# Performance work log

Hardware: AMD Instinct MI355X
Metric: run time of the kernel (lower is better)

The kernel has to match this reference:

```python
import jax, jax.numpy as jnp
import numpy as np

P_EPS = 1e-6            # nn.PairwiseDistance default eps
ALPHA = 0.25
STD_TARGET = 1.0
NUM_COMMUNITIES = 512   # C = number of unique community ids
BIG = 1e30              # masking value for hard-negative min


def setup_inputs() -> dict:
    key = jax.random.key(0)
    k1, k2, k3 = jax.random.split(key, 3)
    B, N, D, C = 1, 100000, 128, NUM_COMMUNITIES
    node_features = jax.random.normal(k1, (B, N, D), dtype=jnp.float32)
    # row 0: a permutation of node indices; row 1: community of that node.
    perm = jax.random.permutation(k2, N).astype(jnp.int32)
    comm_per_node = jnp.concatenate([
        jnp.arange(C, dtype=jnp.int32),  # guarantee every community appears
        jax.random.randint(k3, (N - C,), 0, C, dtype=jnp.int32),
    ])
    community_belong_list = jnp.stack([perm, comm_per_node[perm]])  # [2, N]
    return {"node_features": node_features, "community_belong_list": community_belong_list}


def reference(node_features, community_belong_list):
    B, N, D = node_features.shape
    C = NUM_COMMUNITIES
    dt = node_features.dtype

    # ---- _community_inverse_permute: invert row-0 permutation, reorder columns ----
    perm = community_belong_list[0]
    inv = jnp.zeros((N,), perm.dtype).at[perm].add(jnp.arange(N, dtype=perm.dtype))
    cbl = community_belong_list[:, inv]          # row0 == arange(N) after this
    comm = cbl[1]                                # [N] community id per node
    src = node_features[:, cbl[0], :]            # [B,N,D] gather (identity order)

    # ---- groupby sum / count -> community means ----
    comm_sum = jnp.zeros((B, C, D), dt).at[:, comm, :].add(src)        # [B,C,D]
    counts = jnp.zeros((C,), dt).at[comm].add(jnp.asarray(1.0, dt))   # [C]
    comm_mean = comm_sum / counts[None, :, None]                      # [B,C,D]

    # ---- cdist(node_features, comm_mean, p=2) -> [B,N,C] ----
    x2 = jnp.sum(node_features * node_features, -1)                   # [B,N]
    c2 = jnp.sum(comm_mean * comm_mean, -1)                           # [B,C]
    dots = jnp.einsum('bnd,bcd->bnc', node_features, comm_mean)
    distance = jnp.sqrt(jnp.maximum(x2[:, :, None] + c2[:, None, :] - 2.0 * dots, 0.0))

    # ---- leave-one-out community mean per node, positive distance ----
    cnt_pn = counts[comm]                                             # [N]
    cnt_m1 = jnp.maximum(cnt_pn - 1.0, 1.0)                           # [N]
    x_minus = jnp.where((cnt_pn == 1.0)[None, :, None], jnp.asarray(0.0, dt), src)
    loo_mean = (comm_sum[:, comm, :] - x_minus) / cnt_m1[None, :, None]
    pos_dist = jnp.sqrt(jnp.sum((loo_mean - src + P_EPS) ** 2, -1))   # [B,N]

    # ---- negatives: all communities except the node's own ----
    own = distance[:, jnp.arange(N), comm]                            # [B,N]
    mean_neg = (jnp.sum(distance, -1) - own) / (C - 1)                # [B,N]
    pos_mask = jnp.zeros((N, C), bool).at[jnp.arange(N), comm].set(True)
    hard_neg = jnp.min(jnp.where(pos_mask[None], jnp.asarray(BIG, dt), distance), -1)

    trip_mean = jnp.maximum(pos_dist - mean_neg + ALPHA, 0.0)
    trip_min = jnp.maximum(pos_dist - hard_neg + ALPHA, 0.0)

    # ---- groupby std (unbiased) per community per feature ----
    sq = jnp.zeros((B, C, D), dt).at[:, comm, :].add((src - comm_mean[:, comm, :]) ** 2)
    std = jnp.sqrt(sq / jnp.maximum(counts - 1.0, 1.0)[None, :, None])

    return (trip_mean.mean(), trip_min.mean(), ((std - STD_TARGET) ** 2).mean())
```

## Files before the change

kernel.cpp:

```cpp
#include <hip/hip_runtime.h>

#define NCOMM 512
#define DIM   128
#define ALPHA 0.25f
#define PEPS  1e-6f
#define BIGF  1e30f
#define TILE_C 16
#define NT    (NCOMM / TILE_C)

typedef __attribute__((ext_vector_type(8))) _Float16 f16x8;
typedef __attribute__((ext_vector_type(4))) float f32x4;

#define GLOAD_LDS16(g, l) __builtin_amdgcn_global_load_lds( \
    (const __attribute__((address_space(1))) void*)(g), \
    (__attribute__((address_space(3))) void*)(l), 16, 0, 0)


__global__ void k_prep(const int* __restrict__ cbl, int* __restrict__ comm,
                       int* __restrict__ counts, int N) {
    __shared__ int h[NCOMM];
    int t = threadIdx.x;
    h[t] = 0; h[t + 256] = 0;
    __syncthreads();
    int i = blockIdx.x * 256 + t;
    if (i < N) {
        int p = cbl[i];
        int c = cbl[N + i];
        comm[p] = c;
        atomicAdd(&h[c], 1);
    }
    __syncthreads();
    int v = h[t];        if (v) atomicAdd(&counts[t], v);
    v = h[t + 256];      if (v) atomicAdd(&counts[t + 256], v);
}

__global__ void k_scan(const int* __restrict__ counts, int* __restrict__ offsets,
                       int* __restrict__ cursor, float* __restrict__ countf) {
    __shared__ int sc[NCOMM];
    int t = threadIdx.x;
    int v0 = counts[t];
    sc[t] = v0;
    __syncthreads();
    for (int off = 1; off < NCOMM; off <<= 1) {
        int v = (t >= off) ? sc[t - off] : 0;
        __syncthreads();
        sc[t] += v;
        __syncthreads();
    }
    int excl = sc[t] - v0;
    offsets[t] = excl;
    cursor[t]  = excl;
    countf[t]  = (float)v0;
}

__global__ void k_sort(const int* __restrict__ comm, int* __restrict__ cursor,
                       int* __restrict__ sorted, int N) {
    __shared__ int h[NCOMM], hb[NCOMM];
    int t = threadIdx.x;
    h[t] = 0; h[t + 256] = 0;
    __syncthreads();
    int j0 = blockIdx.x * 1024 + t;
    int cs[4];
    #pragma unroll
    for (int q = 0; q < 4; ++q) {
        int j = j0 + q * 256;
        cs[q] = (j < N) ? comm[j] : -1;
        if (cs[q] >= 0) atomicAdd(&h[cs[q]], 1);
    }
    __syncthreads();
    int v = h[t];        if (v) hb[t] = atomicAdd(&cursor[t], v);
    v = h[t + 256];      if (v) hb[t + 256] = atomicAdd(&cursor[t + 256], v);
    __syncthreads();
    #pragma unroll
    for (int q = 0; q < 4; ++q) {
        int j = j0 + q * 256;
        if (cs[q] >= 0) {
            int p = atomicAdd(&hb[cs[q]], 1);
            sorted[p] = j;
        }
    }
}


__global__ void __launch_bounds__(512) k_stats(
        const float* __restrict__ NF,
        const int* __restrict__ sorted, const int* __restrict__ offsets,
        const int* __restrict__ counts,
        float* __restrict__ comm_sum,
        _Float16* __restrict__ CMh,
        float* __restrict__ c2, float* __restrict__ accum) {
    __shared__ int ridx[512];
    __shared__ float4 bufS[512], bufQ[512];
    int c = blockIdx.x, t = threadIdx.x;
    int d4 = t & 31, r = t >> 5;
    int cnt = counts[c], base = offsets[c];
    const float4* NF4 = (const float4*)NF;

    float4 s4 = make_float4(0.f, 0.f, 0.f, 0.f);
    float4 q4 = make_float4(0.f, 0.f, 0.f, 0.f);
    for (int chunk = 0; chunk < cnt; chunk += 512) {
        int m = min(cnt - chunk, 512);
        for (int i = t; i < m; i += 512) ridx[i] = sorted[base + chunk + i];
        __syncthreads();
        int i = r;
        for (; i + 48 < m; i += 64) {
            int a0 = ridx[i], a1 = ridx[i + 16], a2 = ridx[i + 32], a3 = ridx[i + 48];
            float4 v0 = NF4[(size_t)a0 * 32 + d4];
            float4 v1 = NF4[(size_t)a1 * 32 + d4];
            float4 v2 = NF4[(size_t)a2 * 32 + d4];
            float4 v3 = NF4[(size_t)a3 * 32 + d4];
            s4.x += v0.x; s4.y += v0.y; s4.z += v0.z; s4.w += v0.w;
            q4.x = fmaf(v0.x, v0.x, q4.x); q4.y = fmaf(v0.y, v0.y, q4.y);
            q4.z = fmaf(v0.z, v0.z, q4.z); q4.w = fmaf(v0.w, v0.w, q4.w);
            s4.x += v1.x; s4.y += v1.y; s4.z += v1.z; s4.w += v1.w;
            q4.x = fmaf(v1.x, v1.x, q4.x); q4.y = fmaf(v1.y, v1.y, q4.y);
            q4.z = fmaf(v1.z, v1.z, q4.z); q4.w = fmaf(v1.w, v1.w, q4.w);
            s4.x += v2.x; s4.y += v2.y; s4.z += v2.z; s4.w += v2.w;
            q4.x = fmaf(v2.x, v2.x, q4.x); q4.y = fmaf(v2.y, v2.y, q4.y);
            q4.z = fmaf(v2.z, v2.z, q4.z); q4.w = fmaf(v2.w, v2.w, q4.w);
            s4.x += v3.x; s4.y += v3.y; s4.z += v3.z; s4.w += v3.w;
            q4.x = fmaf(v3.x, v3.x, q4.x); q4.y = fmaf(v3.y, v3.y, q4.y);
            q4.z = fmaf(v3.z, v3.z, q4.z); q4.w = fmaf(v3.w, v3.w, q4.w);
        }
        for (; i < m; i += 16) {
            float4 v = NF4[(size_t)ridx[i] * 32 + d4];
            s4.x += v.x; s4.y += v.y; s4.z += v.z; s4.w += v.w;
            q4.x = fmaf(v.x, v.x, q4.x); q4.y = fmaf(v.y, v.y, q4.y);
            q4.z = fmaf(v.z, v.z, q4.z); q4.w = fmaf(v.w, v.w, q4.w);
        }
        __syncthreads();
    }
    bufS[t] = s4; bufQ[t] = q4;
    __syncthreads();
    if (t < 256) {
        float4 a = bufS[t], b = bufS[t + 256];
        a.x += b.x; a.y += b.y; a.z += b.z; a.w += b.w; bufS[t] = a;
        float4 e = bufQ[t], f = bufQ[t + 256];
        e.x += f.x; e.y += f.y; e.z += f.z; e.w += f.w; bufQ[t] = e;
    }
    __syncthreads();
    if (t < 128) {
        float4 a = bufS[t], b = bufS[t + 128];
        a.x += b.x; a.y += b.y; a.z += b.z; a.w += b.w; bufS[t] = a;
        float4 e = bufQ[t], f = bufQ[t + 128];
        e.x += f.x; e.y += f.y; e.z += f.z; e.w += f.w; bufQ[t] = e;
    }
    __syncthreads();
    if (t < 64) {
        float4 a = bufS[t], b = bufS[t + 64];
        a.x += b.x; a.y += b.y; a.z += b.z; a.w += b.w; bufS[t] = a;
        float4 e = bufQ[t], f = bufQ[t + 64];
        e.x += f.x; e.y += f.y; e.z += f.z; e.w += f.w; bufQ[t] = e;
    }
    __syncthreads();
    if (t < 32) {
        float4 a = bufS[t], b = bufS[t + 32];
        a.x += b.x; a.y += b.y; a.z += b.z; a.w += b.w;
        float4 e = bufQ[t], f = bufQ[t + 32];
        e.x += f.x; e.y += f.y; e.z += f.z; e.w += f.w;
        float sarr[4] = {a.x, a.y, a.z, a.w};
        float qarr[4] = {e.x, e.y, e.z, e.w};
        float cf = (float)cnt;
        float mm = 0.f, ee = 0.f;
        #pragma unroll
        for (int k = 0; k < 4; ++k) {
            int d = t * 4 + k;
            float s = sarr[k];
            comm_sum[c * DIM + d] = s;
            float m = (cnt > 0) ? s / cf : 0.f;
            CMh[c * DIM + d] = (_Float16)m;
            float varn = fmaxf(fmaf(-cf * m, m, qarr[k]), 0.f);
            float stdv = sqrtf(varn / fmaxf(cf - 1.f, 1.f));
            float er = stdv - 1.f;
            mm = fmaf(m, m, mm);
            ee = fmaf(er, er, ee);
        }
        #pragma unroll
        for (int msk = 1; msk < 32; msk <<= 1) {
            mm += __shfl_xor(mm, msk);
            ee += __shfl_xor(ee, msk);
        }
        if (t == 0) {
            c2[c] = mm;
            atomicAdd(&accum[2], ee);
        }
    }
}


__global__ void __launch_bounds__(256, 4) k_main(
        const float* __restrict__ NF,
        const _Float16* __restrict__ CMh,
        const float* __restrict__ comm_sum,
        const float* __restrict__ c2g,
        const float* __restrict__ countf,
        const int* __restrict__ comm,
        float* __restrict__ accum, int N) {
    __shared__ _Float16 Bst[4][4][TILE_C * 64];
    __shared__ float c2s[NCOMM];
    __shared__ int   comms[128];
    __shared__ float x2sh[128];
    __shared__ float sums[128], mins[128];
    __shared__ float red[8];

    int tid = threadIdx.x;
    int w  = tid >> 6;
    int l  = tid & 63;
    int lr = l & 15;
    int lk = l >> 4;
    int n0 = blockIdx.x * 128;

    int off0 = ((l >> 3) << 7) + (((l & 7) ^ ((l >> 3) & 7)) << 3);
    const _Float16* gsrc = CMh + off0;
    auto stage = [&](int ss, int b) {
        const _Float16* g = gsrc + (size_t)(ss >> 1) * 2048 + (ss & 1) * 64;
        _Float16* lh = &Bst[w][b][0];
        GLOAD_LDS16(g,        lh);
        GLOAD_LDS16(g + 1024, lh + 512);
    };
    stage(0, 0); stage(1, 1); stage(2, 2);

    c2s[tid]       = c2g[tid];
    c2s[tid + 256] = c2g[tid + 256];
    if (tid < 128) {
        int gn = n0 + tid;
        comms[tid] = (gn < N) ? comm[gn] : -1;
    }

    f16x8 ah[2][4];
    #pragma unroll
    for (int mf = 0; mf < 2; ++mf) {
        int n = n0 + w * 32 + mf * 16 + lr;
        const float4* src = (const float4*)NF + (size_t)n * 32 + lk * 2;
        float p2 = 0.f;
        #pragma unroll
        for (int ks = 0; ks < 4; ++ks) {
            float4 v0 = make_float4(0.f, 0.f, 0.f, 0.f), v1 = v0;
            if (n < N) { v0 = src[ks * 8]; v1 = src[ks * 8 + 1]; }
            float fr[8] = {v0.x, v0.y, v0.z, v0.w, v1.x, v1.y, v1.z, v1.w};
            f16x8 hh;
            #pragma unroll
            for (int t = 0; t < 8; ++t) {
                hh[t] = (_Float16)fr[t];
                p2 = fmaf(fr[t], fr[t], p2);
            }
            ah[mf][ks] = hh;
        }
        p2 += __shfl_xor(p2, 16);
        p2 += __shfl_xor(p2, 32);
        if (lk == 0) x2sh[w * 32 + mf * 16 + lr] = -0.5f * p2;
    }
    __syncthreads();

    f32x4 x2v[2];
    int cnv[2][4];
    float sumv[2][4], minv[2][4];
    #pragma unroll
    for (int mf = 0; mf < 2; ++mf) {
        x2v[mf] = *(const f32x4*)&x2sh[w * 32 + mf * 16 + lk * 4];
        #pragma unroll
        for (int j = 0; j < 4; ++j) {
            cnv[mf][j] = comms[w * 32 + mf * 16 + lk * 4 + j];
            sumv[mf][j] = 0.f; minv[mf][j] = BIGF;
        }
    }

    for (int tt = 0; tt < NT; ++tt) {
        f32x4 acc0, acc1;
        {
            int ssn = 2 * tt + 3;
            if (ssn < 64) stage(ssn, ssn & 3);
            if (tt <= 30) { asm volatile("s_waitcnt vmcnt(6)" ::: "memory"); }
            else          { asm volatile("s_waitcnt vmcnt(2)" ::: "memory"); }
            __builtin_amdgcn_sched_barrier(0);
            const _Float16* bp = &Bst[w][(2 * tt) & 3][0];
            acc0 = x2v[0]; acc1 = x2v[1];
            #pragma unroll
            for (int ks2 = 0; ks2 < 2; ++ks2) {
                int ch = (ks2 * 4 + lk) ^ (lr & 7);
                f16x8 b = *(const f16x8*)&bp[(size_t)(lr * 64 + ch * 8)];
                acc0 = __builtin_amdgcn_mfma_f32_16x16x32_f16(ah[0][ks2], b, acc0, 0, 0, 0);
                acc1 = __builtin_amdgcn_mfma_f32_16x16x32_f16(ah[1][ks2], b, acc1, 0, 0, 0);
            }
        }
        {
            int ssn = 2 * tt + 4;
            if (ssn < 64) stage(ssn, ssn & 3);
            if (tt <= 29)      { asm volatile("s_waitcnt vmcnt(6)" ::: "memory"); }
            else if (tt == 30) { asm volatile("s_waitcnt vmcnt(4)" ::: "memory"); }
            else               { asm volatile("s_waitcnt vmcnt(0)" ::: "memory"); }
            __builtin_amdgcn_sched_barrier(0);
            const _Float16* bp = &Bst[w][(2 * tt + 1) & 3][0];
            #pragma unroll
            for (int ks2 = 0; ks2 < 2; ++ks2) {
                int ch = (ks2 * 4 + lk) ^ (lr & 7);
                f16x8 b = *(const f16x8*)&bp[(size_t)(lr * 64 + ch * 8)];
                acc0 = __builtin_amdgcn_mfma_f32_16x16x32_f16(ah[0][2 + ks2], b, acc0, 0, 0, 0);
                acc1 = __builtin_amdgcn_mfma_f32_16x16x32_f16(ah[1][2 + ks2], b, acc1, 0, 0, 0);
            }
            int ccol = tt * TILE_C + lr;
            float c2v = c2s[ccol];
            #pragma unroll
            for (int j = 0; j < 4; ++j) {
                float d2a = fmaf(-2.f, acc0[j], c2v);
                float da  = __builtin_amdgcn_sqrtf(fmaxf(d2a, 0.f));
                sumv[0][j] += da;
                minv[0][j] = fminf(minv[0][j], (cnv[0][j] == ccol) ? BIGF : da);
                float d2b = fmaf(-2.f, acc1[j], c2v);
                float db  = __builtin_amdgcn_sqrtf(fmaxf(d2b, 0.f));
                sumv[1][j] += db;
                minv[1][j] = fminf(minv[1][j], (cnv[1][j] == ccol) ? BIGF : db);
            }
        }
    }

    #pragma unroll
    for (int mf = 0; mf < 2; ++mf)
        #pragma unroll
        for (int j = 0; j < 4; ++j) {
            float sv = sumv[mf][j], mv = minv[mf][j];
            #pragma unroll
            for (int msk = 1; msk < 16; msk <<= 1) {
                sv += __shfl_xor(sv, msk);
                mv = fminf(mv, __shfl_xor(mv, msk));
            }
            if (lr == 0) {
                int idx = w * 32 + mf * 16 + lk * 4 + j;
                sums[idx] = sv; mins[idx] = mv;
            }
        }
    __syncthreads();

    float tmean = 0.f, tminv = 0.f;
    {
        int ln = tid >> 1, half = tid & 1;
        int n = n0 + ln;
        if (n < N) {
            int cnode = comms[ln];
            float cf  = countf[cnode];
            float cm1 = fmaxf(cf - 1.f, 1.f);
            float rs  = 1.f / cm1;
            bool single = (cf == 1.f);
            const float4* srow = (const float4*)NF + (size_t)n * 32 + half * 16;
            const float4* csum = (const float4*)(comm_sum + (size_t)cnode * DIM) + half * 16;
            float q = 0.f, dot = 0.f;
            #pragma unroll
            for (int m = 0; m < 16; ++m) {
                float4 sv = srow[m];
                float4 cs = csum[m];
                float4 xm = single ? make_float4(0.f, 0.f, 0.f, 0.f) : sv;
                float lx = (cs.x - xm.x) * rs - sv.x + PEPS;
                float ly = (cs.y - xm.y) * rs - sv.y + PEPS;
                float lz = (cs.z - xm.z) * rs - sv.z + PEPS;
                float lw = (cs.w - xm.w) * rs - sv.w + PEPS;
                q = fmaf(lx, lx, fmaf(ly, ly, fmaf(lz, lz, fmaf(lw, lw, q))));
                dot = fmaf(sv.x, cs.x, fmaf(sv.y, cs.y, fmaf(sv.z, cs.z, fmaf(sv.w, cs.w, dot))));
            }
            q   += __shfl_xor(q, 1);
            dot += __shfl_xor(dot, 1);
            if (half == 0) {
                float pos = sqrtf(q);
                float x2 = -2.f * x2sh[ln];
                float ownd2 = x2 + c2s[cnode] - 2.f * (dot / cf);
                float own = sqrtf(fmaxf(ownd2, 0.f));
                float mean_neg = (sums[ln] - own) * (1.f / (float)(NCOMM - 1));
                tmean = fmaxf(pos - mean_neg + ALPHA, 0.f);
                tminv = fmaxf(pos - mins[ln] + ALPHA, 0.f);
            }
        }
    }
    #pragma unroll
    for (int msk = 1; msk < 64; msk <<= 1) {
        tmean += __shfl_xor(tmean, msk);
        tminv += __shfl_xor(tminv, msk);
    }
    if ((tid & 63) == 0) { red[w * 2] = tmean; red[w * 2 + 1] = tminv; }
    __syncthreads();
    if (tid == 0) {
        atomicAdd(&accum[0], red[0] + red[2] + red[4] + red[6]);
        atomicAdd(&accum[1], red[1] + red[3] + red[5] + red[7]);
    }
}

__global__ void k_final(const float* __restrict__ accum, float* __restrict__ out, int N) {
    if (threadIdx.x == 0) {
        out[0] = accum[0] / (float)N;
        out[1] = accum[1] / (float)N;
        out[2] = accum[2] / (float)(NCOMM * DIM);
    }
}


extern "C" void kernel_launch(void* const* d_in, const int* in_sizes, int n_in,
                              void* d_out, int out_size, void* d_ws, size_t ws_size,
                              hipStream_t stream) {
    const float* NF  = (const float*)d_in[0];
    const int*   CBL = (const int*)d_in[1];
    int N = in_sizes[1] / 2;
    if (N <= 0) return;

    char* ws = (char*)d_ws;
    float* accum   = (float*)ws;
    int*   counts  = (int*)(ws + 16);
    int*   cursor  = (int*)(ws + 16 + 2048);
    int*   offsets = (int*)(ws + 16 + 2 * 2048);
    float* countf  = (float*)(ws + 16 + 3 * 2048);
    float* c2      = (float*)(ws + 16 + 4 * 2048);
    char* p = ws + 16 + 5 * 2048;
    int* comm   = (int*)p; p += (size_t)N * 4;
    int* sorted = (int*)p; p += (size_t)N * 4;
    float* comm_sum = (float*)p; p += (size_t)NCOMM * DIM * 4;
    _Float16* CMh = (_Float16*)p;

    hipMemsetAsync(d_ws, 0, 16 + 2048, stream);

    int nb = (N + 255) / 256;
    k_prep<<<nb, 256, 0, stream>>>(CBL, comm, counts, N);
    k_scan<<<1, NCOMM, 0, stream>>>(counts, offsets, cursor, countf);
    int nb4 = (N + 1023) / 1024;
    k_sort<<<nb4, 256, 0, stream>>>(comm, cursor, sorted, N);
    k_stats<<<NCOMM, 512, 0, stream>>>(NF, sorted, offsets, counts,
                                       comm_sum, CMh, c2, accum);
    int mb = (N + 127) / 128;
    k_main<<<mb, 256, 0, stream>>>(NF, CMh, comm_sum, c2, countf,
                                   comm, accum, N);
    k_final<<<1, 64, 0, stream>>>(accum, (float*)d_out, N);
}
```

Measured before the change: 119.7 us.

## Make k_main persistent with register-resident centroids and double-buffered node tiles

Turns k_main into a persistent kernel of 256 blocks with 1024 threads each. Each of the 16 waves keeps its own 32-community slice of the fp16 centroid matrix in registers. Node tiles of 64 rows are staged through double-buffered LDS, with the next tile prefetched while the current one is processed. The goal is to stop re-streaming all 512 centroids from global memory to LDS for every 128-node block. The cost is an extra cross-wave partial-sum reduction through LDS and two block barriers per tile. Launch_bounds(1024,4) also puts pressure on registers and occupancy.

```diff
diff --git a/kernel.cpp b/kernel.cpp
--- a/kernel.cpp
+++ b/kernel.cpp
@@ -5,15 +5,9 @@
 #define ALPHA 0.25f
 #define PEPS  1e-6f
 #define BIGF  1e30f
-#define TILE_C 16
-#define NT    (NCOMM / TILE_C)
 
 typedef __attribute__((ext_vector_type(8))) _Float16 f16x8;
 typedef __attribute__((ext_vector_type(4))) float f32x4;
-
-#define GLOAD_LDS16(g, l) __builtin_amdgcn_global_load_lds( \
-    (const __attribute__((address_space(1))) void*)(g), \
-    (__attribute__((address_space(3))) void*)(l), 16, 0, 0)
 
 
 __global__ void k_prep(const int* __restrict__ cbl, int* __restrict__ comm,
@@ -188,7 +182,7 @@
 }
 
 
-__global__ void __launch_bounds__(256, 4) k_main(
+__global__ void __launch_bounds__(1024, 4) k_main(
         const float* __restrict__ NF,
         const _Float16* __restrict__ CMh,
         const float* __restrict__ comm_sum,
@@ -196,189 +190,193 @@
         const float* __restrict__ countf,
         const int* __restrict__ comm,
         float* __restrict__ accum, int N) {
-    __shared__ _Float16 Bst[4][4][TILE_C * 64];
+    __shared__ _Float16 Ast[2][64 * DIM];
+    __shared__ float part_s[64][16];
+    __shared__ float part_m[64][16];
     __shared__ float c2s[NCOMM];
-    __shared__ int   comms[128];
-    __shared__ float x2sh[128];
-    __shared__ float sums[128], mins[128];
-    __shared__ float red[8];
+    __shared__ float x2t[2][64];
+    __shared__ int   comt[2][64];
+    __shared__ float red[32];
 
     int tid = threadIdx.x;
     int w  = tid >> 6;
     int l  = tid & 63;
     int lr = l & 15;
     int lk = l >> 4;
-    int n0 = blockIdx.x * 128;
-
-    int off0 = ((l >> 3) << 7) + (((l & 7) ^ ((l >> 3) & 7)) << 3);
-    const _Float16* gsrc = CMh + off0;
-    auto stage = [&](int ss, int b) {
-        const _Float16* g = gsrc + (size_t)(ss >> 1) * 2048 + (ss & 1) * 64;
-        _Float16* lh = &Bst[w][b][0];
-        GLOAD_LDS16(g,        lh);
-        GLOAD_LDS16(g + 1024, lh + 512);
-    };
-    stage(0, 0); stage(1, 1); stage(2, 2);
-
-    c2s[tid]       = c2g[tid];
-    c2s[tid + 256] = c2g[tid + 256];
-    if (tid < 128) {
-        int gn = n0 + tid;
-        comms[tid] = (gn < N) ? comm[gn] : -1;
-    }
-
-    f16x8 ah[2][4];
+    int row = tid >> 4;
+    int cq  = tid & 15;
+    int TT  = (N + 63) >> 6;
+
+    f16x8 bh[2][4];
     #pragma unroll
-    for (int mf = 0; mf < 2; ++mf) {
-        int n = n0 + w * 32 + mf * 16 + lr;
-        const float4* src = (const float4*)NF + (size_t)n * 32 + lk * 2;
-        float p2 = 0.f;
-        #pragma unroll
-        for (int ks = 0; ks < 4; ++ks) {
-            float4 v0 = make_float4(0.f, 0.f, 0.f, 0.f), v1 = v0;
-            if (n < N) { v0 = src[ks * 8]; v1 = src[ks * 8 + 1]; }
-            float fr[8] = {v0.x, v0.y, v0.z, v0.w, v1.x, v1.y, v1.z, v1.w};
-            f16x8 hh;
+    for (int s = 0; s < 2; ++s) {
+        int c0 = w * 32 + s * 16;
+        #pragma unroll
+        for (int ks = 0; ks < 4; ++ks)
+            bh[s][ks] = *(const f16x8*)&CMh[(size_t)(c0 + lr) * DIM + ks * 32 + lk * 8];
+    }
+    if (tid < NCOMM) c2s[tid] = c2g[tid];
+
+    {
+        int n = blockIdx.x * 64 + row;
+        const float4* base = (const float4*)NF + (size_t)n * 32 + cq * 2;
+        float4 v0 = make_float4(0.f, 0.f, 0.f, 0.f), v1 = v0;
+        int cm = -1;
+        if (n < N) { v0 = base[0]; v1 = base[1]; cm = comm[n]; }
+        float fr[8] = {v0.x, v0.y, v0.z, v0.w, v1.x, v1.y, v1.z, v1.w};
+        f16x8 hh; float p2 = 0.f;
+        #pragma unroll
+        for (int u = 0; u < 8; ++u) { hh[u] = (_Float16)fr[u]; p2 = fmaf(fr[u], fr[u], p2); }
+        *(f16x8*)&Ast[0][row * DIM + ((cq ^ (row & 7)) * 8)] = hh;
+        p2 += __shfl_xor(p2, 1); p2 += __shfl_xor(p2, 2);
+        p2 += __shfl_xor(p2, 4); p2 += __shfl_xor(p2, 8);
+        if (cq == 0) x2t[0][row] = -0.5f * p2;
+        if (cq == 1) comt[0][row] = cm;
+    }
+    __syncthreads();
+
+    float tmean = 0.f, tminv = 0.f;
+    int cur = 0;
+    for (int t = blockIdx.x; t < TT; t += 256) {
+        int tn = t + 256;
+        bool hasNext = tn < TT;
+        float4 nv0 = make_float4(0.f, 0.f, 0.f, 0.f), nv1 = nv0;
+        int ncm = -1;
+        if (hasNext) {
+            int n = tn * 64 + row;
+            const float4* base = (const float4*)NF + (size_t)n * 32 + cq * 2;
+            if (n < N) { nv0 = base[0]; nv1 = base[1]; ncm = comm[n]; }
+        }
+
+        float sumv[4][4], minv[4][4];
+        #pragma unroll
+        for (int nf = 0; nf < 4; ++nf)
             #pragma unroll
-            for (int t = 0; t < 8; ++t) {
-                hh[t] = (_Float16)fr[t];
-                p2 = fmaf(fr[t], fr[t], p2);
+            for (int j = 0; j < 4; ++j) { sumv[nf][j] = 0.f; minv[nf][j] = BIGF; }
+
+        const _Float16* Ab = &Ast[cur][0];
+        #pragma unroll
+        for (int nf = 0; nf < 4; ++nf) {
+            int rbase = (nf * 16 + lr) * DIM;
+            f16x8 ah0 = *(const f16x8*)&Ab[rbase + (((0 + lk) ^ (lr & 7)) * 8)];
+            f16x8 ah1 = *(const f16x8*)&Ab[rbase + (((4 + lk) ^ (lr & 7)) * 8)];
+            f16x8 ah2 = *(const f16x8*)&Ab[rbase + (((8 + lk) ^ (lr & 7)) * 8)];
+            f16x8 ah3 = *(const f16x8*)&Ab[rbase + (((12 + lk) ^ (lr & 7)) * 8)];
+            f32x4 x2v = *(const f32x4*)&x2t[cur][nf * 16 + lk * 4];
+            int4  cn  = *(const int4*)&comt[cur][nf * 16 + lk * 4];
+            #pragma unroll
+            for (int s = 0; s < 2; ++s) {
+                f32x4 acc = x2v;
+                acc = __builtin_amdgcn_mfma_f32_16x16x32_f16(ah0, bh[s][0], acc, 0, 0, 0);
+                acc = __builtin_amdgcn_mfma_f32_16x16x32_f16(ah1, bh[s][1], acc, 0, 0, 0);
+                acc = __builtin_amdgcn_mfma_f32_16x16x32_f16(ah2, bh[s][2], acc, 0, 0, 0);
+                acc = __builtin_amdgcn_mfma_f32_16x16x32_f16(ah3, bh[s][3], acc, 0, 0, 0);
+                int ccol = w * 32 + s * 16 + lr;
+                float c2v = c2s[ccol];
+                int cna[4] = {cn.x, cn.y, cn.z, cn.w};
+                #pragma unroll
+                for (int j = 0; j < 4; ++j) {
+                    float d2 = fmaf(-2.f, acc[j], c2v);
+                    float da = __builtin_amdgcn_sqrtf(fmaxf(d2, 0.f));
+                    sumv[nf][j] += da;
+                    minv[nf][j] = fminf(minv[nf][j], (cna[j] == ccol) ? BIGF : da);
+                }
             }
-            ah[mf][ks] = hh;
-        }
-        p2 += __shfl_xor(p2, 16);
-        p2 += __shfl_xor(p2, 32);
-        if (lk == 0) x2sh[w * 32 + mf * 16 + lr] = -0.5f * p2;
-    }
-    __syncthreads();
-
-    f32x4 x2v[2];
-    int cnv[2][4];
-    float sumv[2][4], minv[2][4];
-    #pragma unroll
-    for (int mf = 0; mf < 2; ++mf) {
-        x2v[mf] = *(const f32x4*)&x2sh[w * 32 + mf * 16 + lk * 4];
-        #pragma unroll
-        for (int j = 0; j < 4; ++j) {
-            cnv[mf][j] = comms[w * 32 + mf * 16 + lk * 4 + j];
-            sumv[mf][j] = 0.f; minv[mf][j] = BIGF;
-        }
-    }
-
-    for (int tt = 0; tt < NT; ++tt) {
-        f32x4 acc0, acc1;
-        {
-            int ssn = 2 * tt + 3;
-            if (ssn < 64) stage(ssn, ssn & 3);
-            if (tt <= 30) { asm volatile("s_waitcnt vmcnt(6)" ::: "memory"); }
-            else          { asm volatile("s_waitcnt vmcnt(2)" ::: "memory"); }
-            __builtin_amdgcn_sched_barrier(0);
-            const _Float16* bp = &Bst[w][(2 * tt) & 3][0];
-            acc0 = x2v[0]; acc1 = x2v[1];
-            #pragma unroll
-            for (int ks2 = 0; ks2 < 2; ++ks2) {
-                int ch = (ks2 * 4 + lk) ^ (lr & 7);
-                f16x8 b = *(const f16x8*)&bp[(size_t)(lr * 64 + ch * 8)];
-                acc0 = __builtin_amdgcn_mfma_f32_16x16x32_f16(ah[0][ks2], b, acc0, 0, 0, 0);
-                acc1 = __builtin_amdgcn_mfma_f32_16x16x32_f16(ah[1][ks2], b, acc1, 0, 0, 0);
-            }
-        }
-        {
-            int ssn = 2 * tt + 4;
-            if (ssn < 64) stage(ssn, ssn & 3);
-            if (tt <= 29)      { asm volatile("s_waitcnt vmcnt(6)" ::: "memory"); }
-            else if (tt == 30) { asm volatile("s_waitcnt vmcnt(4)" ::: "memory"); }
-            else               { asm volatile("s_waitcnt vmcnt(0)" ::: "memory"); }
-            __builtin_amdgcn_sched_barrier(0);
-            const _Float16* bp = &Bst[w][(2 * tt + 1) & 3][0];
-            #pragma unroll
-            for (int ks2 = 0; ks2 < 2; ++ks2) {
-                int ch = (ks2 * 4 + lk) ^ (lr & 7);
-                f16x8 b = *(const f16x8*)&bp[(size_t)(lr * 64 + ch * 8)];
-                acc0 = __builtin_amdgcn_mfma_f32_16x16x32_f16(ah[0][2 + ks2], b, acc0, 0, 0, 0);
-                acc1 = __builtin_amdgcn_mfma_f32_16x16x32_f16(ah[1][2 + ks2], b, acc1, 0, 0, 0);
-            }
-            int ccol = tt * TILE_C + lr;
-            float c2v = c2s[ccol];
+        }
+        #pragma unroll
+        for (int nf = 0; nf < 4; ++nf)
             #pragma unroll
             for (int j = 0; j < 4; ++j) {
-                float d2a = fmaf(-2.f, acc0[j], c2v);
-                float da  = __builtin_amdgcn_sqrtf(fmaxf(d2a, 0.f));
-                sumv[0][j] += da;
-                minv[0][j] = fminf(minv[0][j], (cnv[0][j] == ccol) ? BIGF : da);
-                float d2b = fmaf(-2.f, acc1[j], c2v);
-                float db  = __builtin_amdgcn_sqrtf(fmaxf(d2b, 0.f));
-                sumv[1][j] += db;
-                minv[1][j] = fminf(minv[1][j], (cnv[1][j] == ccol) ? BIGF : db);
+                float sv = sumv[nf][j], mv = minv[nf][j];
+                #pragma unroll
+                for (int msk = 1; msk < 16; msk <<= 1) {
+                    sv += __shfl_xor(sv, msk);
+                    mv = fminf(mv, __shfl_xor(mv, msk));
+                }
+                if (lr == 0) {
+                    int r2 = nf * 16 + lk * 4 + j;
+                    part_s[r2][w] = sv;
+                    part_m[r2][w] = mv;
+                }
             }
-        }
-    }
-
-    #pragma unroll
-    for (int mf = 0; mf < 2; ++mf)
-        #pragma unroll
-        for (int j = 0; j < 4; ++j) {
-            float sv = sumv[mf][j], mv = minv[mf][j];
+
+        if (hasNext) {
+            float fr[8] = {nv0.x, nv0.y, nv0.z, nv0.w, nv1.x, nv1.y, nv1.z, nv1.w};
+            f16x8 hh; float p2 = 0.f;
+            #pragma unroll
+            for (int u = 0; u < 8; ++u) { hh[u] = (_Float16)fr[u]; p2 = fmaf(fr[u], fr[u], p2); }
+            int b = cur ^ 1;
+            *(f16x8*)&Ast[b][row * DIM + ((cq ^ (row & 7)) * 8)] = hh;
+            p2 += __shfl_xor(p2, 1); p2 += __shfl_xor(p2, 2);
+            p2 += __shfl_xor(p2, 4); p2 += __shfl_xor(p2, 8);
+            if (cq == 0) x2t[b][row] = -0.5f * p2;
+            if (cq == 1) comt[b][row] = ncm;
+        }
+        __syncthreads();
+
+        {
+            float s  = part_s[row][cq];
+            float mn = part_m[row][cq];
             #pragma unroll
             for (int msk = 1; msk < 16; msk <<= 1) {
-                sv += __shfl_xor(sv, msk);
-                mv = fminf(mv, __shfl_xor(mv, msk));
+                s += __shfl_xor(s, msk);
+                mn = fminf(mn, __shfl_xor(mn, msk));
             }
-            if (lr == 0) {
-                int idx = w * 32 + mf * 16 + lk * 4 + j;
-                sums[idx] = sv; mins[idx] = mv;
+            int n = t * 64 + row;
+            if (n < N) {
+                int cnode = comt[cur][row];
+                float cf  = countf[cnode];
+                float cm1 = fmaxf(cf - 1.f, 1.f);
+                float rs  = 1.f / cm1;
+                bool single = (cf == 1.f);
+                const float4* srow = (const float4*)NF + (size_t)n * 32 + cq * 2;
+                const float4* csum = (const float4*)(comm_sum + (size_t)cnode * DIM) + cq * 2;
+                float q = 0.f, dot = 0.f;
+                #pragma unroll
+                for (int m2 = 0; m2 < 2; ++m2) {
+                    float4 sv = srow[m2];
+                    float4 cs = csum[m2];
+                    float4 xm = single ? make_float4(0.f, 0.f, 0.f, 0.f) : sv;
+                    float lx = (cs.x - xm.x) * rs - sv.x + PEPS;
+                    float ly = (cs.y - xm.y) * rs - sv.y + PEPS;
+                    float lz = (cs.z - xm.z) * rs - sv.z + PEPS;
+                    float lw = (cs.w - xm.w) * rs - sv.w + PEPS;
+                    q = fmaf(lx, lx, fmaf(ly, ly, fmaf(lz, lz, fmaf(lw, lw, q))));
+                    dot = fmaf(sv.x, cs.x, fmaf(sv.y, cs.y, fmaf(sv.z, cs.z, fmaf(sv.w, cs.w, dot))));
+                }
+                #pragma unroll
+                for (int msk = 1; msk < 16; msk <<= 1) {
+                    q   += __shfl_xor(q, msk);
+                    dot += __shfl_xor(dot, msk);
+                }
+                if (cq == 0) {
+                    float pos = sqrtf(q);
+                    float x2 = -2.f * x2t[cur][row];
+                    float ownd2 = x2 + c2s[cnode] - 2.f * (dot / cf);
+                    float own = sqrtf(fmaxf(ownd2, 0.f));
+                    float mean_neg = (s - own) * (1.f / (float)(NCOMM - 1));
+                    tmean += fmaxf(pos - mean_neg + ALPHA, 0.f);
+                    tminv += fmaxf(pos - mn + ALPHA, 0.f);
+                }
             }
         }
-    __syncthreads();
-
-    float tmean = 0.f, tminv = 0.f;
-    {
-        int ln = tid >> 1, half = tid & 1;
-        int n = n0 + ln;
-        if (n < N) {
-            int cnode = comms[ln];
-            float cf  = countf[cnode];
-            float cm1 = fmaxf(cf - 1.f, 1.f);
-            float rs  = 1.f / cm1;
-            bool single = (cf == 1.f);
-            const float4* srow = (const float4*)NF + (size_t)n * 32 + half * 16;
-            const float4* csum = (const float4*)(comm_sum + (size_t)cnode * DIM) + half * 16;
-            float q = 0.f, dot = 0.f;
-            #pragma unroll
-            for (int m = 0; m < 16; ++m) {
-                float4 sv = srow[m];
-                float4 cs = csum[m];
-                float4 xm = single ? make_float4(0.f, 0.f, 0.f, 0.f) : sv;
-                float lx = (cs.x - xm.x) * rs - sv.x + PEPS;
-                float ly = (cs.y - xm.y) * rs - sv.y + PEPS;
-                float lz = (cs.z - xm.z) * rs - sv.z + PEPS;
-                float lw = (cs.w - xm.w) * rs - sv.w + PEPS;
-                q = fmaf(lx, lx, fmaf(ly, ly, fmaf(lz, lz, fmaf(lw, lw, q))));
-                dot = fmaf(sv.x, cs.x, fmaf(sv.y, cs.y, fmaf(sv.z, cs.z, fmaf(sv.w, cs.w, dot))));
-            }
-            q   += __shfl_xor(q, 1);
-            dot += __shfl_xor(dot, 1);
-            if (half == 0) {
-                float pos = sqrtf(q);
-                float x2 = -2.f * x2sh[ln];
-                float ownd2 = x2 + c2s[cnode] - 2.f * (dot / cf);
-                float own = sqrtf(fmaxf(ownd2, 0.f));
-                float mean_neg = (sums[ln] - own) * (1.f / (float)(NCOMM - 1));
-                tmean = fmaxf(pos - mean_neg + ALPHA, 0.f);
-                tminv = fmaxf(pos - mins[ln] + ALPHA, 0.f);
-            }
-        }
-    }
+        __syncthreads();
+        cur ^= 1;
+    }
+
     #pragma unroll
     for (int msk = 1; msk < 64; msk <<= 1) {
         tmean += __shfl_xor(tmean, msk);
         tminv += __shfl_xor(tminv, msk);
     }
-    if ((tid & 63) == 0) { red[w * 2] = tmean; red[w * 2 + 1] = tminv; }
+    if (l == 0) { red[w * 2] = tmean; red[w * 2 + 1] = tminv; }
     __syncthreads();
     if (tid == 0) {
-        atomicAdd(&accum[0], red[0] + red[2] + red[4] + red[6]);
-        atomicAdd(&accum[1], red[1] + red[3] + red[5] + red[7]);
+        float a0 = 0.f, a1 = 0.f;
+        #pragma unroll
+        for (int i = 0; i < 16; ++i) { a0 += red[i * 2]; a1 += red[i * 2 + 1]; }
+        atomicAdd(&accum[0], a0);
+        atomicAdd(&accum[1], a1);
     }
 }
 
@@ -421,8 +419,7 @@
     k_sort<<<nb4, 256, 0, stream>>>(comm, cursor, sorted, N);
     k_stats<<<NCOMM, 512, 0, stream>>>(NF, sorted, offsets, counts,
                                        comm_sum, CMh, c2, accum);
-    int mb = (N + 127) / 128;
-    k_main<<<mb, 256, 0, stream>>>(NF, CMh, comm_sum, c2, countf,
-                                   comm, accum, N);
+    k_main<<<256, 1024, 0, stream>>>(NF, CMh, comm_sum, c2, countf,
+                                     comm, accum, N);
     k_final<<<1, 64, 0, stream>>>(accum, (float*)d_out, N);
 }
```

Measured after the change: 127.6 us. 1.07x slower.
